# Kernel optimization log

Measured on AMD Instinct MI355X. Metric: run time of the kernel, lower is better.

Reference implementation:

```python
import jax, jax.numpy as jnp
import numpy as np

N_NODES = 40000
N_EDGES = 640000
DIM = 128
N_BASIS = 50
N_FILTERS = 128
CUTOFF = 5.0
LOG2 = float(np.log(2.0))
PI = float(np.pi)


def ssp(t):
    # ShiftedSoftplus: softplus(x) - log(2), numerically stable via logaddexp
    return jnp.logaddexp(t, 0.0) - LOG2


def setup_inputs() -> dict:
    key = jax.random.key(0)
    ks = jax.random.split(key, 16)
    u = lambda k, shape, fan_in: jax.random.uniform(k, shape, jnp.float32, -1.0, 1.0) / np.sqrt(fan_in)
    return {
        "x": jax.random.normal(ks[0], (N_NODES, DIM), jnp.float32),
        "r_ij": jax.random.uniform(ks[1], (N_EDGES,), jnp.float32) * CUTOFF,
        "f_ij": jax.random.normal(ks[2], (N_EDGES, N_BASIS), jnp.float32),
        "ind_i": jax.random.randint(ks[3], (N_EDGES,), 0, N_NODES),
        "ind_j": jax.random.randint(ks[4], (N_EDGES,), 0, N_NODES),
        # parameters
        "W_in2f": u(ks[5], (DIM, N_FILTERS), DIM),            # Linear(dim, n_filters, bias=False)
        "W_f1": u(ks[6], (N_BASIS, N_FILTERS), N_BASIS),       # filter_network Linear 1
        "b_f1": u(ks[7], (N_FILTERS,), N_BASIS),
        "W_f2": u(ks[8], (N_FILTERS, N_FILTERS), N_FILTERS),   # filter_network Linear 2
        "b_f2": u(ks[9], (N_FILTERS,), N_FILTERS),
        "W_out": u(ks[10], (N_FILTERS, DIM), N_FILTERS),       # f2out Linear
        "b_out": u(ks[11], (DIM,), N_FILTERS),
        "W_lin": u(ks[12], (DIM, DIM), DIM),                   # final lin
        "b_lin": u(ks[13], (DIM,), DIM),
    }


def reference(x, r_ij, f_ij, ind_i, ind_j,
              W_in2f, W_f1, b_f1, W_f2, b_f2, W_out, b_out, W_lin, b_lin):
    # filter network: Linear -> ShiftedSoftplus -> Linear, on edges: [E, nf]
    W = ssp(f_ij @ W_f1 + b_f1) @ W_f2 + b_f2
    # cosine cutoff: [E]
    C = 0.5 * (jnp.cos(r_ij * (PI / CUTOFF)) + 1.0) * (r_ij < CUTOFF).astype(r_ij.dtype)
    W = W * C[:, None]
    # node embedding -> filters: [N, nf]
    h = x @ W_in2f
    # gather source nodes, modulate by filters: [E, nf]
    msg = h[ind_j] * W
    # scatter-add pool to destination nodes: [N, nf]
    agg = jax.ops.segment_sum(msg, ind_i, num_segments=x.shape[0])
    # f2out: Linear -> ShiftedSoftplus, then final Linear
    v = ssp(agg @ W_out + b_out)
    return v @ W_lin + b_lin
```

## Files before the change

kernel.cpp:

```cpp
#include <hip/hip_runtime.h>
#include <hip/hip_fp16.h>

#define N_NODES_C 40000
#define N_EDGES_C 640000
#define DIM 128
#define NB 50
#define LDA 132
#define BLK 256
#define TROWS 64
#define LOG2_C 0.6931471805599453f
#define PI_OVER_CUT 0.6283185307179586f
#define NSCAN_BLK 157

typedef __attribute__((ext_vector_type(8))) short s8v;
typedef __attribute__((ext_vector_type(4))) float f4v;

#define MFMA_BF16 __builtin_amdgcn_mfma_f32_16x16x32_bf16

#define SEG_IN2F_H 0
#define SEG_IN2F_L 20480
#define SEG_F1_H   40960
#define SEG_F1_L   51200
#define SEG_F2_H   61440
#define SEG_F2_L   81920
#define SEG_OUT_H  102400
#define SEG_OUT_L  122880
#define SEG_LIN_H  143360
#define SEG_LIN_L  163840
#define WSPLIT_USHORTS 184320

__device__ __forceinline__ unsigned short f2bf(float x) {
    unsigned int u = __float_as_uint(x);
    u += 0x7fffu + ((u >> 16) & 1u);
    return (unsigned short)(u >> 16);
}
__device__ __forceinline__ float bf2f(unsigned short h) {
    return __uint_as_float(((unsigned int)h) << 16);
}
__device__ __forceinline__ float ssp_f(float t) {
    float e = __expf(-fabsf(t));
    return fmaxf(t, 0.0f) + __logf(1.0f + e) - LOG2_C;
}
__device__ __forceinline__ void split8t(const float* av, s8v& Ah, s8v& Al) {
#pragma unroll
    for (int j = 0; j < 8; j += 2) {
        unsigned int u0 = __float_as_uint(av[j]);
        unsigned int u1 = __float_as_uint(av[j + 1]);
        float h0 = __uint_as_float(u0 & 0xffff0000u);
        float h1 = __uint_as_float(u1 & 0xffff0000u);
        unsigned int r0 = __float_as_uint(av[j] - h0);
        unsigned int r1 = __float_as_uint(av[j + 1] - h1);
        ((unsigned int*)&Ah)[j >> 1] = __builtin_amdgcn_perm(u1, u0, 0x07060302);
        ((unsigned int*)&Al)[j >> 1] = __builtin_amdgcn_perm(r1, r0, 0x07060302);
    }
}
__device__ __forceinline__ void mfma4x2(const unsigned short* __restrict__ bh,
                                        const unsigned short* __restrict__ bl,
                                        const s8v& Ah0, const s8v& Al0,
                                        const s8v& Ah1, const s8v& Al1,
                                        f4v acc0[4], f4v acc1[4]) {
    s8v B[4];
#pragma unroll
    for (int t = 0; t < 4; ++t) B[t] = *(const s8v*)(bl + t * 640);
#pragma unroll
    for (int t = 0; t < 4; ++t) {
        acc0[t] = MFMA_BF16(Ah0, B[t], acc0[t], 0, 0, 0);
        acc1[t] = MFMA_BF16(Ah1, B[t], acc1[t], 0, 0, 0);
    }
#pragma unroll
    for (int t = 0; t < 4; ++t) B[t] = *(const s8v*)(bh + t * 640);
#pragma unroll
    for (int t = 0; t < 4; ++t) {
        acc0[t] = MFMA_BF16(Al0, B[t], acc0[t], 0, 0, 0);
        acc0[t] = MFMA_BF16(Ah0, B[t], acc0[t], 0, 0, 0);
        acc1[t] = MFMA_BF16(Al1, B[t], acc1[t], 0, 0, 0);
        acc1[t] = MFMA_BF16(Ah1, B[t], acc1[t], 0, 0, 0);
    }
}

__global__ __launch_bounds__(BLK) void split5_kernel(const float* __restrict__ Wa,
                                                     const float* __restrict__ Wb,
                                                     const float* __restrict__ Wc,
                                                     const float* __restrict__ Wd,
                                                     const float* __restrict__ We,
                                                     unsigned short* __restrict__ Ws) {
    int i = blockIdx.x * BLK + threadIdx.x;
    if (i >= 18 * 4096) return;
    int chunk = i >> 12, r = i & 4095, k = r & 31, col = r >> 5;
    const float* W; int Kr, ck, hb, lb;
    if (chunk < 4)       { W = Wa; Kr = 128; ck = chunk;      hb = SEG_IN2F_H; lb = SEG_IN2F_L; }
    else if (chunk < 6)  { W = Wb; Kr = 50;  ck = chunk - 4;  hb = SEG_F1_H;   lb = SEG_F1_L; }
    else if (chunk < 10) { W = Wc; Kr = 128; ck = chunk - 6;  hb = SEG_F2_H;   lb = SEG_F2_L; }
    else if (chunk < 14) { W = Wd; Kr = 128; ck = chunk - 10; hb = SEG_OUT_H;  lb = SEG_OUT_L; }
    else                 { W = We; Kr = 128; ck = chunk - 14; hb = SEG_LIN_H;  lb = SEG_LIN_L; }
    int krow = ck * 32 + k;
    float v = (krow < Kr) ? W[(size_t)krow * DIM + col] : 0.f;
    unsigned short h16 = f2bf(v);
    int o = ck * 5120 + col * 40 + k;
    Ws[hb + o] = h16;
    Ws[lb + o] = f2bf(v - bf2f(h16));
}

__global__ __launch_bounds__(BLK, 4) void node_in2f_mfma(const float* __restrict__ x,
                                                         const unsigned short* __restrict__ Ws,
                                                         float* __restrict__ h) {
    const int tid = threadIdx.x;
    const int w = tid >> 6, l = tid & 63, lr = l & 15, lk = l >> 4;
    const int rpair = w & 1, colbase = (w >> 1) * 64;
    const int n0 = blockIdx.x * TROWS;
    const int rowA0 = rpair * 32 + lr, rowA1 = rowA0 + 16;
    const float* xr0 = x + (size_t)(n0 + rowA0) * DIM;
    const float* xr1 = x + (size_t)(n0 + rowA1) * DIM;

    f4v acc0[4], acc1[4];
#pragma unroll
    for (int t = 0; t < 4; ++t) {
        acc0[t] = (f4v){0.f, 0.f, 0.f, 0.f};
        acc1[t] = (f4v){0.f, 0.f, 0.f, 0.f};
    }
#pragma unroll
    for (int kc = 0; kc < 4; ++kc) {
        const float* ap0 = xr0 + kc * 32 + lk * 8;
        const float* ap1 = xr1 + kc * 32 + lk * 8;
        float4 a0 = *(const float4*)ap0, a1 = *(const float4*)(ap0 + 4);
        float4 b0 = *(const float4*)ap1, b1 = *(const float4*)(ap1 + 4);
        float av0[8] = {a0.x, a0.y, a0.z, a0.w, a1.x, a1.y, a1.z, a1.w};
        float av1[8] = {b0.x, b0.y, b0.z, b0.w, b1.x, b1.y, b1.z, b1.w};
        s8v Ah0, Al0, Ah1, Al1;
        split8t(av0, Ah0, Al0);
        split8t(av1, Ah1, Al1);
        const int bo = kc * 5120 + (colbase + lr) * 40 + lk * 8;
        mfma4x2(Ws + SEG_IN2F_H + bo, Ws + SEG_IN2F_L + bo, Ah0, Al0, Ah1, Al1, acc0, acc1);
    }
#pragma unroll
    for (int t = 0; t < 4; ++t)
#pragma unroll
        for (int r = 0; r < 4; ++r) {
            int col = colbase + t * 16 + lr;
            h[(size_t)(n0 + rpair * 32 + lk * 4 + r) * DIM + col] = acc0[t][r];
            h[(size_t)(n0 + rpair * 32 + 16 + lk * 4 + r) * DIM + col] = acc1[t][r];
        }
}

__global__ __launch_bounds__(BLK) void hist_kernel(const int* __restrict__ ind_i,
                                                   int* __restrict__ cnt) {
    int e = blockIdx.x * BLK + threadIdx.x;
    if (e < N_EDGES_C) atomicAdd(&cnt[ind_i[e]], 1);
}

__global__ __launch_bounds__(BLK) void scan1_kernel(const int* __restrict__ cnt,
                                                    int* __restrict__ excl,
                                                    int* __restrict__ bsum) {
    __shared__ int s[BLK];
    const int tid = threadIdx.x;
    const int idx = blockIdx.x * BLK + tid;
    int v = (idx < N_NODES_C) ? cnt[idx] : 0;
    s[tid] = v;
    __syncthreads();
    for (int off = 1; off < BLK; off <<= 1) {
        int t = (tid >= off) ? s[tid - off] : 0;
        __syncthreads();
        s[tid] += t;
        __syncthreads();
    }
    if (idx < N_NODES_C) excl[idx] = s[tid] - v;
    if (tid == BLK - 1) bsum[blockIdx.x] = s[tid];
}

__global__ __launch_bounds__(BLK) void scan2_kernel(int* __restrict__ bsum) {
    __shared__ int s[BLK];
    const int tid = threadIdx.x;
    int v = (tid < NSCAN_BLK) ? bsum[tid] : 0;
    s[tid] = v;
    __syncthreads();
    for (int off = 1; off < BLK; off <<= 1) {
        int t = (tid >= off) ? s[tid - off] : 0;
        __syncthreads();
        s[tid] += t;
        __syncthreads();
    }
    if (tid < NSCAN_BLK) bsum[tid] = s[tid] - v;
}

__global__ __launch_bounds__(BLK) void scan3_kernel(int* __restrict__ start,
                                                    int* __restrict__ cursor,
                                                    const int* __restrict__ bsum) {
    const int idx = blockIdx.x * BLK + threadIdx.x;
    if (idx < N_NODES_C) {
        int v = start[idx] + bsum[blockIdx.x];
        start[idx] = v;
        cursor[idx] = v;
    }
}

__global__ __launch_bounds__(BLK) void place_kernel(const int* __restrict__ ind_i,
                                                    int* __restrict__ cursor,
                                                    int* __restrict__ pos) {
    int e = blockIdx.x * BLK + threadIdx.x;
    if (e < N_EDGES_C) {
        int slot = atomicAdd(&cursor[ind_i[e]], 1);
        pos[e] = slot;
    }
}

__global__ __launch_bounds__(BLK, 4) void edge_kernel_mfma(const float* __restrict__ f_ij,
                                                           const float* __restrict__ r_ij,
                                                           const int* __restrict__ ind_j,
                                                           const int* __restrict__ pos,
                                                           const unsigned short* __restrict__ Ws,
                                                           const float* __restrict__ b_f1,
                                                           const float* __restrict__ b_f2,
                                                           const float* __restrict__ h,
                                                           __half* __restrict__ msg) {
    __shared__ __align__(16) char smem[34816];
    unsigned short* t1h = (unsigned short*)smem;
    unsigned short* t1l = t1h + 64 * 136;
    float* tf = (float*)smem;

    const int tid = threadIdx.x;
    const int w = tid >> 6, l = tid & 63, lr = l & 15, lk = l >> 4;
    const int rt = tid >> 4, ct = tid & 15;
    const int rpair = w & 1, colbase = (w >> 1) * 64;
    const int e0 = blockIdx.x * TROWS;
    const int rowA0 = rpair * 32 + lr, rowA1 = rowA0 + 16;

    f4v acc0[4], acc1[4];
#pragma unroll
    for (int t = 0; t < 4; ++t) {
        float bv = b_f1[colbase + t * 16 + lr];
        acc0[t] = (f4v){bv, bv, bv, bv};
        acc1[t] = (f4v){bv, bv, bv, bv};
    }
    const float* fr0 = f_ij + (size_t)(e0 + rowA0) * NB;
    const float* fr1 = f_ij + (size_t)(e0 + rowA1) * NB;
#pragma unroll
    for (int kc = 0; kc < 2; ++kc) {
        int kb = kc * 32 + lk * 8;
        float av0[8], av1[8];
#pragma unroll
        for (int ii = 0; ii < 4; ++ii) {
            int k = kb + ii * 2;
            float2 v0 = (k < NB) ? *(const float2*)(fr0 + k) : make_float2(0.f, 0.f);
            float2 v1 = (k < NB) ? *(const float2*)(fr1 + k) : make_float2(0.f, 0.f);
            av0[ii * 2] = v0.x; av0[ii * 2 + 1] = v0.y;
            av1[ii * 2] = v1.x; av1[ii * 2 + 1] = v1.y;
        }
        s8v Ah0, Al0, Ah1, Al1;
        split8t(av0, Ah0, Al0);
        split8t(av1, Ah1, Al1);
        const int bo = kc * 5120 + (colbase + lr) * 40 + lk * 8;
        mfma4x2(Ws + SEG_F1_H + bo, Ws + SEG_F1_L + bo, Ah0, Al0, Ah1, Al1, acc0, acc1);
    }
#pragma unroll
    for (int t = 0; t < 4; ++t)
#pragma unroll
        for (int r = 0; r < 4; ++r) {
            int col = colbase + t * 16 + lr;
            {
                float v = ssp_f(acc0[t][r]);
                unsigned int u = __float_as_uint(v);
                float hf = __uint_as_float(u & 0xffff0000u);
                int idx = (rpair * 32 + lk * 4 + r) * 136 + col;
                t1h[idx] = (unsigned short)(u >> 16);
                t1l[idx] = (unsigned short)(__float_as_uint(v - hf) >> 16);
            }
            {
                float v = ssp_f(acc1[t][r]);
                unsigned int u = __float_as_uint(v);
                float hf = __uint_as_float(u & 0xffff0000u);
                int idx = (rpair * 32 + 16 + lk * 4 + r) * 136 + col;
                t1h[idx] = (unsigned short)(u >> 16);
                t1l[idx] = (unsigned short)(__float_as_uint(v - hf) >> 16);
            }
        }
    __syncthreads();

#pragma unroll
    for (int t = 0; t < 4; ++t) {
        float bv = b_f2[colbase + t * 16 + lr];
        acc0[t] = (f4v){bv, bv, bv, bv};
        acc1[t] = (f4v){bv, bv, bv, bv};
    }
#pragma unroll
    for (int kc = 0; kc < 4; ++kc) {
        s8v Ah0 = *(const s8v*)&t1h[rowA0 * 136 + kc * 32 + lk * 8];
        s8v Al0 = *(const s8v*)&t1l[rowA0 * 136 + kc * 32 + lk * 8];
        s8v Ah1 = *(const s8v*)&t1h[rowA1 * 136 + kc * 32 + lk * 8];
        s8v Al1 = *(const s8v*)&t1l[rowA1 * 136 + kc * 32 + lk * 8];
        const int bo = kc * 5120 + (colbase + lr) * 40 + lk * 8;
        mfma4x2(Ws + SEG_F2_H + bo, Ws + SEG_F2_L + bo, Ah0, Al0, Ah1, Al1, acc0, acc1);
    }
    __syncthreads();
#pragma unroll
    for (int t = 0; t < 4; ++t)
#pragma unroll
        for (int r = 0; r < 4; ++r) {
            int col = colbase + t * 16 + lr;
            tf[(rpair * 32 + lk * 4 + r) * LDA + col] = acc0[t][r];
            tf[(rpair * 32 + 16 + lk * 4 + r) * LDA + col] = acc1[t][r];
        }
    __syncthreads();

#pragma unroll
    for (int i = 0; i < 4; ++i) {
        int e = e0 + rt * 4 + i;
        float rr = r_ij[e];
        float C = (rr < 5.0f) ? (0.5f * __cosf(rr * PI_OVER_CUT) + 0.5f) : 0.0f;
        int nj = ind_j[e];
        const float* hp = &h[(size_t)nj * DIM + ct * 8];
        float4 h0 = *(const float4*)hp, h1 = *(const float4*)(hp + 4);
        const float* ep = &tf[(rt * 4 + i) * LDA + ct * 8];
        float4 a0 = *(const float4*)ep, a1 = *(const float4*)(ep + 4);
        __half2 o0 = __floats2half2_rn(h0.x * a0.x * C, h0.y * a0.y * C);
        __half2 o1 = __floats2half2_rn(h0.z * a0.z * C, h0.w * a0.w * C);
        __half2 o2 = __floats2half2_rn(h1.x * a1.x * C, h1.y * a1.y * C);
        __half2 o3 = __floats2half2_rn(h1.z * a1.z * C, h1.w * a1.w * C);
        __half* mp = &msg[(size_t)pos[e] * DIM + ct * 8];
        *(uint4*)mp = make_uint4(*(unsigned int*)&o0, *(unsigned int*)&o1,
                                 *(unsigned int*)&o2, *(unsigned int*)&o3);
    }
}

__global__ __launch_bounds__(BLK) void gather_kernel(const __half* __restrict__ msg,
                                                     const int* __restrict__ start,
                                                     const int* __restrict__ cnt,
                                                     float* __restrict__ agg) {
    const int wave = threadIdx.x >> 6;
    const int lane = threadIdx.x & 63;
    const int node = blockIdx.x * 4 + wave;
    if (node >= N_NODES_C) return;
    const int s = start[node];
    const int d = cnt[node];
    const __half* base = msg + (size_t)s * DIM + lane * 2;
    float ax = 0.f, ay = 0.f;
    int k = 0;
    for (; k + 1 < d; k += 2) {
        float2 fa = __half22float2(*(const __half2*)(base + (size_t)k * DIM));
        float2 fb = __half22float2(*(const __half2*)(base + (size_t)(k + 1) * DIM));
        ax += fa.x + fb.x;
        ay += fa.y + fb.y;
    }
    if (k < d) {
        float2 fa = __half22float2(*(const __half2*)(base + (size_t)k * DIM));
        ax += fa.x;
        ay += fa.y;
    }
    *(float2*)&agg[(size_t)node * DIM + lane * 2] = make_float2(ax, ay);
}

__global__ __launch_bounds__(BLK, 4) void node_out_mfma(const float* __restrict__ agg,
                                                        const unsigned short* __restrict__ Ws,
                                                        const float* __restrict__ b_out,
                                                        const float* __restrict__ b_lin,
                                                        float* __restrict__ out) {
    __shared__ __align__(16) char smem[34816];
    unsigned short* t1h = (unsigned short*)smem;
    unsigned short* t1l = t1h + 64 * 136;

    const int tid = threadIdx.x;
    const int w = tid >> 6, l = tid & 63, lr = l & 15, lk = l >> 4;
    const int rpair = w & 1, colbase = (w >> 1) * 64;
    const int n0 = blockIdx.x * TROWS;
    const int rowA0 = rpair * 32 + lr, rowA1 = rowA0 + 16;
    const float* ar0 = agg + (size_t)(n0 + rowA0) * DIM;
    const float* ar1 = agg + (size_t)(n0 + rowA1) * DIM;

    f4v acc0[4], acc1[4];
#pragma unroll
    for (int t = 0; t < 4; ++t) {
        float bv = b_out[colbase + t * 16 + lr];
        acc0[t] = (f4v){bv, bv, bv, bv};
        acc1[t] = (f4v){bv, bv, bv, bv};
    }
#pragma unroll
    for (int kc = 0; kc < 4; ++kc) {
        const float* ap0 = ar0 + kc * 32 + lk * 8;
        const float* ap1 = ar1 + kc * 32 + lk * 8;
        float4 a0 = *(const float4*)ap0, a1 = *(const float4*)(ap0 + 4);
        float4 b0 = *(const float4*)ap1, b1 = *(const float4*)(ap1 + 4);
        float av0[8] = {a0.x, a0.y, a0.z, a0.w, a1.x, a1.y, a1.z, a1.w};
        float av1[8] = {b0.x, b0.y, b0.z, b0.w, b1.x, b1.y, b1.z, b1.w};
        s8v Ah0, Al0, Ah1, Al1;
        split8t(av0, Ah0, Al0);
        split8t(av1, Ah1, Al1);
        const int bo = kc * 5120 + (colbase + lr) * 40 + lk * 8;
        mfma4x2(Ws + SEG_OUT_H + bo, Ws + SEG_OUT_L + bo, Ah0, Al0, Ah1, Al1, acc0, acc1);
    }
#pragma unroll
    for (int t = 0; t < 4; ++t)
#pragma unroll
        for (int r = 0; r < 4; ++r) {
            int col = colbase + t * 16 + lr;
            {
                float v = ssp_f(acc0[t][r]);
                unsigned int u = __float_as_uint(v);
                float hf = __uint_as_float(u & 0xffff0000u);
                int idx = (rpair * 32 + lk * 4 + r) * 136 + col;
                t1h[idx] = (unsigned short)(u >> 16);
                t1l[idx] = (unsigned short)(__float_as_uint(v - hf) >> 16);
            }
            {
                float v = ssp_f(acc1[t][r]);
                unsigned int u = __float_as_uint(v);
                float hf = __uint_as_float(u & 0xffff0000u);
                int idx = (rpair * 32 + 16 + lk * 4 + r) * 136 + col;
                t1h[idx] = (unsigned short)(u >> 16);
                t1l[idx] = (unsigned short)(__float_as_uint(v - hf) >> 16);
            }
        }
    __syncthreads();

#pragma unroll
    for (int t = 0; t < 4; ++t) {
        float bv = b_lin[colbase + t * 16 + lr];
        acc0[t] = (f4v){bv, bv, bv, bv};
        acc1[t] = (f4v){bv, bv, bv, bv};
    }
#pragma unroll
    for (int kc = 0; kc < 4; ++kc) {
        s8v Ah0 = *(const s8v*)&t1h[rowA0 * 136 + kc * 32 + lk * 8];
        s8v Al0 = *(const s8v*)&t1l[rowA0 * 136 + kc * 32 + lk * 8];
        s8v Ah1 = *(const s8v*)&t1h[rowA1 * 136 + kc * 32 + lk * 8];
        s8v Al1 = *(const s8v*)&t1l[rowA1 * 136 + kc * 32 + lk * 8];
        const int bo = kc * 5120 + (colbase + lr) * 40 + lk * 8;
        mfma4x2(Ws + SEG_LIN_H + bo, Ws + SEG_LIN_L + bo, Ah0, Al0, Ah1, Al1, acc0, acc1);
    }
#pragma unroll
    for (int t = 0; t < 4; ++t)
#pragma unroll
        for (int r = 0; r < 4; ++r) {
            int col = colbase + t * 16 + lr;
            out[(size_t)(n0 + rpair * 32 + lk * 4 + r) * DIM + col] = acc0[t][r];
            out[(size_t)(n0 + rpair * 32 + 16 + lk * 4 + r) * DIM + col] = acc1[t][r];
        }
}

__device__ __forceinline__ void stage_chunk(const float* __restrict__ B, int k0, int rows,
                                            float* __restrict__ Bc, int tid) {
    const int n4 = rows * (DIM / 4);
    const float4* Bg = (const float4*)B + (size_t)k0 * (DIM / 4);
    float4* Bc4 = (float4*)Bc;
    for (int i = tid; i < n4; i += BLK) Bc4[i] = Bg[i];
}

__device__ __forceinline__ void init_acc_bias(float acc[4][8], const float* __restrict__ b, int ct) {
    float4 bb0 = *(const float4*)&b[ct * 8];
    float4 bb1 = *(const float4*)&b[ct * 8 + 4];
#pragma unroll
    for (int i = 0; i < 4; ++i) {
        acc[i][0] = bb0.x; acc[i][1] = bb0.y; acc[i][2] = bb0.z; acc[i][3] = bb0.w;
        acc[i][4] = bb1.x; acc[i][5] = bb1.y; acc[i][6] = bb1.z; acc[i][7] = bb1.w;
    }
}

template <int KPAD>
__device__ __forceinline__ void gemm_tile(const float* __restrict__ A_lds, int lda,
                                          const float* __restrict__ Bglob,
                                          float* __restrict__ Bc,
                                          float acc[4][8], int rt, int ct, int tid) {
    for (int k0 = 0; k0 < KPAD; k0 += 32) {
        __syncthreads();
        stage_chunk(Bglob, k0, 32, Bc, tid);
        __syncthreads();
#pragma unroll 2
        for (int k4 = 0; k4 < 8; ++k4) {
            float4 av[4];
#pragma unroll
            for (int i = 0; i < 4; ++i)
                av[i] = *(const float4*)&A_lds[(rt * 4 + i) * lda + k0 + k4 * 4];
#pragma unroll
            for (int kk = 0; kk < 4; ++kk) {
                const float* bp = &Bc[(k4 * 4 + kk) * DIM + ct * 8];
                float4 b0 = *(const float4*)bp;
                float4 b1 = *(const float4*)(bp + 4);
#pragma unroll
                for (int i = 0; i < 4; ++i) {
                    float a = ((const float*)&av[i])[kk];
                    acc[i][0] = fmaf(a, b0.x, acc[i][0]);
                    acc[i][1] = fmaf(a, b0.y, acc[i][1]);
                    acc[i][2] = fmaf(a, b0.z, acc[i][2]);
                    acc[i][3] = fmaf(a, b0.w, acc[i][3]);
                    acc[i][4] = fmaf(a, b1.x, acc[i][4]);
                    acc[i][5] = fmaf(a, b1.y, acc[i][5]);
                    acc[i][6] = fmaf(a, b1.z, acc[i][6]);
                    acc[i][7] = fmaf(a, b1.w, acc[i][7]);
                }
            }
        }
    }
}

template <int NK2>
__device__ __forceinline__ void gemm1_direct(const float* const (&frow)[4], int k2base,
                                             const float* __restrict__ Bc,
                                             float acc[4][8], int ct) {
#pragma unroll 4
    for (int k2 = 0; k2 < NK2; ++k2) {
        float2 a2[4];
#pragma unroll
        for (int i = 0; i < 4; ++i)
            a2[i] = *(const float2*)(frow[i] + (k2base + k2) * 2);
#pragma unroll
        for (int kk = 0; kk < 2; ++kk) {
            const float* bp = &Bc[(k2 * 2 + kk) * DIM + ct * 8];
            float4 b0 = *(const float4*)bp;
            float4 b1 = *(const float4*)(bp + 4);
#pragma unroll
            for (int i = 0; i < 4; ++i) {
                float a = kk ? a2[i].y : a2[i].x;
                acc[i][0] = fmaf(a, b0.x, acc[i][0]);
                acc[i][1] = fmaf(a, b0.y, acc[i][1]);
                acc[i][2] = fmaf(a, b0.z, acc[i][2]);
                acc[i][3] = fmaf(a, b0.w, acc[i][3]);
                acc[i][4] = fmaf(a, b1.x, acc[i][4]);
                acc[i][5] = fmaf(a, b1.y, acc[i][5]);
                acc[i][6] = fmaf(a, b1.z, acc[i][6]);
                acc[i][7] = fmaf(a, b1.w, acc[i][7]);
            }
        }
    }
}

__global__ __launch_bounds__(BLK) void node_in2f_fb(const float* __restrict__ x,
                                                    const float* __restrict__ W,
                                                    float* __restrict__ h) {
    __shared__ float At[TROWS * LDA];
    __shared__ float Bc[32 * DIM];
    const int tid = threadIdx.x;
    const int rt = tid >> 4, ct = tid & 15;
    const int n0 = blockIdx.x * TROWS;
    for (int i = tid; i < TROWS * (DIM / 4); i += BLK) {
        int row = i >> 5, c4 = i & 31;
        *(float4*)&At[row * LDA + c4 * 4] = *(const float4*)&x[(size_t)(n0 + row) * DIM + c4 * 4];
    }
    float acc[4][8];
#pragma unroll
    for (int i = 0; i < 4; ++i)
#pragma unroll
        for (int j = 0; j < 8; ++j) acc[i][j] = 0.f;
    gemm_tile<DIM>(At, LDA, W, Bc, acc, rt, ct, tid);
#pragma unroll
    for (int i = 0; i < 4; ++i) {
        float* hp = &h[(size_t)(n0 + rt * 4 + i) * DIM + ct * 8];
        *(float4*)hp = make_float4(acc[i][0], acc[i][1], acc[i][2], acc[i][3]);
        *(float4*)(hp + 4) = make_float4(acc[i][4], acc[i][5], acc[i][6], acc[i][7]);
    }
}

__global__ __launch_bounds__(BLK) void node_out_fb(const float* __restrict__ agg,
                                                   const float* __restrict__ W_out,
                                                   const float* __restrict__ b_out,
                                                   const float* __restrict__ W_lin,
                                                   const float* __restrict__ b_lin,
                                                   float* __restrict__ out) {
    __shared__ float At[TROWS * LDA];
    __shared__ float Bc[32 * DIM];
    const int tid = threadIdx.x;
    const int rt = tid >> 4, ct = tid & 15;
    const int n0 = blockIdx.x * TROWS;
    for (int i = tid; i < TROWS * (DIM / 4); i += BLK) {
        int row = i >> 5, c4 = i & 31;
        *(float4*)&At[row * LDA + c4 * 4] = *(const float4*)&agg[(size_t)(n0 + row) * DIM + c4 * 4];
    }
    float acc[4][8];
    init_acc_bias(acc, b_out, ct);
    gemm_tile<DIM>(At, LDA, W_out, Bc, acc, rt, ct, tid);
    __syncthreads();
#pragma unroll
    for (int i = 0; i < 4; ++i) {
        float* tp = &At[(rt * 4 + i) * LDA + ct * 8];
        *(float4*)tp = make_float4(ssp_f(acc[i][0]), ssp_f(acc[i][1]),
                                   ssp_f(acc[i][2]), ssp_f(acc[i][3]));
        *(float4*)(tp + 4) = make_float4(ssp_f(acc[i][4]), ssp_f(acc[i][5]),
                                         ssp_f(acc[i][6]), ssp_f(acc[i][7]));
    }
    init_acc_bias(acc, b_lin, ct);
    gemm_tile<DIM>(At, LDA, W_lin, Bc, acc, rt, ct, tid);
#pragma unroll
    for (int i = 0; i < 4; ++i) {
        float* op = &out[(size_t)(n0 + rt * 4 + i) * DIM + ct * 8];
        *(float4*)op = make_float4(acc[i][0], acc[i][1], acc[i][2], acc[i][3]);
        *(float4*)(op + 4) = make_float4(acc[i][4], acc[i][5], acc[i][6], acc[i][7]);
    }
}

__global__ __launch_bounds__(BLK) void edge_kernel_atomic(const float* __restrict__ f_ij,
                                                          const float* __restrict__ r_ij,
                                                          const int* __restrict__ ind_i,
                                                          const int* __restrict__ ind_j,
                                                          const float* __restrict__ W_f1,
                                                          const float* __restrict__ b_f1,
                                                          const float* __restrict__ W_f2,
                                                          const float* __restrict__ b_f2,
                                                          const float* __restrict__ h,
                                                          float* __restrict__ agg) {
    __shared__ float t1[TROWS * LDA];
    __shared__ float Bc[32 * DIM];
    const int tid = threadIdx.x;
    const int rt = tid >> 4, ct = tid & 15;
    const int e0 = blockIdx.x * TROWS;
    const float* frow[4];
#pragma unroll
    for (int i = 0; i < 4; ++i) frow[i] = f_ij + (size_t)(e0 + rt * 4 + i) * NB;
    float acc[4][8];
    init_acc_bias(acc, b_f1, ct);
    stage_chunk(W_f1, 0, 32, Bc, tid);
    __syncthreads();
    gemm1_direct<16>(frow, 0, Bc, acc, ct);
    __syncthreads();
    stage_chunk(W_f1, 32, 18, Bc, tid);
    __syncthreads();
    gemm1_direct<9>(frow, 16, Bc, acc, ct);
#pragma unroll
    for (int i = 0; i < 4; ++i) {
        float* tp = &t1[(rt * 4 + i) * LDA + ct * 8];
        *(float4*)tp = make_float4(ssp_f(acc[i][0]), ssp_f(acc[i][1]),
                                   ssp_f(acc[i][2]), ssp_f(acc[i][3]));
        *(float4*)(tp + 4) = make_float4(ssp_f(acc[i][4]), ssp_f(acc[i][5]),
                                         ssp_f(acc[i][6]), ssp_f(acc[i][7]));
    }
    init_acc_bias(acc, b_f2, ct);
    gemm_tile<DIM>(t1, LDA, W_f2, Bc, acc, rt, ct, tid);
#pragma unroll
    for (int i = 0; i < 4; ++i) {
        int e = e0 + rt * 4 + i;
        float r = r_ij[e];
        float C = (r < 5.0f) ? 0.5f * (cosf(r * PI_OVER_CUT) + 1.0f) : 0.0f;
        int nj = ind_j[e];
        int ni = ind_i[e];
        const float* hp = &h[(size_t)nj * DIM + ct * 8];
        float4 h0 = *(const float4*)hp;
        float4 h1 = *(const float4*)(hp + 4);
        float* ap = &agg[(size_t)ni * DIM + ct * 8];
        atomicAdd(ap + 0, h0.x * acc[i][0] * C);
        atomicAdd(ap + 1, h0.y * acc[i][1] * C);
        atomicAdd(ap + 2, h0.z * acc[i][2] * C);
        atomicAdd(ap + 3, h0.w * acc[i][3] * C);
        atomicAdd(ap + 4, h1.x * acc[i][4] * C);
        atomicAdd(ap + 5, h1.y * acc[i][5] * C);
        atomicAdd(ap + 6, h1.z * acc[i][6] * C);
        atomicAdd(ap + 7, h1.w * acc[i][7] * C);
    }
}

extern "C" void kernel_launch(void* const* d_in, const int* in_sizes, int n_in,
                              void* d_out, int out_size, void* d_ws, size_t ws_size,
                              hipStream_t stream) {
    const float* x      = (const float*)d_in[0];
    const float* r_ij   = (const float*)d_in[1];
    const float* f_ij   = (const float*)d_in[2];
    const int*   ind_i  = (const int*)d_in[3];
    const int*   ind_j  = (const int*)d_in[4];
    const float* W_in2f = (const float*)d_in[5];
    const float* W_f1   = (const float*)d_in[6];
    const float* b_f1   = (const float*)d_in[7];
    const float* W_f2   = (const float*)d_in[8];
    const float* b_f2   = (const float*)d_in[9];
    const float* W_out  = (const float*)d_in[10];
    const float* b_out  = (const float*)d_in[11];
    const float* W_lin  = (const float*)d_in[12];
    const float* b_lin  = (const float*)d_in[13];
    float* out = (float*)d_out;

    char* ws = (char*)d_ws;
    size_t off = 0;
    auto alloc = [&](size_t bytes) {
        char* p = ws + off;
        off = (off + bytes + 511) & ~(size_t)511;
        return p;
    };
    unsigned short* Wsplit = (unsigned short*)alloc(WSPLIT_USHORTS * sizeof(unsigned short));
    float*  h      = (float*)alloc((size_t)N_NODES_C * DIM * sizeof(float));
    float*  agg    = (float*)alloc((size_t)N_NODES_C * DIM * sizeof(float));
    __half* msg    = (__half*)alloc((size_t)N_EDGES_C * DIM * sizeof(__half));
    int*    pos    = (int*)alloc((size_t)N_EDGES_C * sizeof(int));
    int*    cnt    = (int*)alloc((size_t)N_NODES_C * sizeof(int));
    int*    startA = (int*)alloc((size_t)N_NODES_C * sizeof(int));
    int*    cursor = (int*)alloc((size_t)N_NODES_C * sizeof(int));
    int*    bsum   = (int*)alloc((size_t)NSCAN_BLK * sizeof(int));
    const bool have_ws = (off <= ws_size);

    if (have_ws) {
        split5_kernel<<<(18 * 4096 + BLK - 1) / BLK, BLK, 0, stream>>>(
            W_in2f, W_f1, W_f2, W_out, W_lin, Wsplit);

        node_in2f_mfma<<<N_NODES_C / TROWS, BLK, 0, stream>>>(x, Wsplit, h);

        hipMemsetAsync(cnt, 0, (size_t)N_NODES_C * sizeof(int), stream);
        hist_kernel<<<(N_EDGES_C + BLK - 1) / BLK, BLK, 0, stream>>>(ind_i, cnt);
        scan1_kernel<<<NSCAN_BLK, BLK, 0, stream>>>(cnt, startA, bsum);
        scan2_kernel<<<1, BLK, 0, stream>>>(bsum);
        scan3_kernel<<<NSCAN_BLK, BLK, 0, stream>>>(startA, cursor, bsum);
        place_kernel<<<(N_EDGES_C + BLK - 1) / BLK, BLK, 0, stream>>>(ind_i, cursor, pos);

        edge_kernel_mfma<<<N_EDGES_C / TROWS, BLK, 0, stream>>>(
            f_ij, r_ij, ind_j, pos, Wsplit, b_f1, b_f2, h, msg);
        gather_kernel<<<(N_NODES_C + 3) / 4, BLK, 0, stream>>>(msg, startA, cnt, agg);

        node_out_mfma<<<N_NODES_C / TROWS, BLK, 0, stream>>>(agg, Wsplit, b_out, b_lin, out);
    } else {
        float* h2   = (float*)d_ws;
        float* agg2 = h2 + (size_t)N_NODES_C * DIM;
        node_in2f_fb<<<N_NODES_C / TROWS, BLK, 0, stream>>>(x, W_in2f, h2);
        hipMemsetAsync(agg2, 0, (size_t)N_NODES_C * DIM * sizeof(float), stream);
        edge_kernel_atomic<<<N_EDGES_C / TROWS, BLK, 0, stream>>>(
            f_ij, r_ij, ind_i, ind_j, W_f1, b_f1, W_f2, b_f2, h2, agg2);
        node_out_fb<<<N_NODES_C / TROWS, BLK, 0, stream>>>(agg2, W_out, b_out, W_lin, b_lin, out);
    }
}
```

Before: 308.4 us.

## Fuse gather into node output kernel and software-pipeline B loads in edge GEMMs

Removes the separate gather kernel and the fp32 agg buffer. The node output kernel now sums each node's fp16 messages directly into LDS as split bf16 tiles and then runs both GEMMs on them. The edge kernel double-buffers the weight fragment loads across k-chunks and issues the r_ij, ind_j, pos and h gathers earlier so they overlap with the MFMA work. The cost is higher register pressure and a gather loop inside a GEMM kernel, where 16 threads serialize each node's message sum and degree imbalance can stall the block.

Result: faster. 298.4 us (-3.2%).

```diff
diff --git a/kernel.cpp b/kernel.cpp
--- a/kernel.cpp
+++ b/kernel.cpp
@@ -54,28 +54,101 @@
         ((unsigned int*)&Al)[j >> 1] = __builtin_amdgcn_perm(r1, r0, 0x07060302);
     }
 }
+__device__ __forceinline__ void f2x4_to_split(const float2 v[4], s8v& Ah, s8v& Al) {
+    float av[8] = {v[0].x, v[0].y, v[1].x, v[1].y, v[2].x, v[2].y, v[3].x, v[3].y};
+    split8t(av, Ah, Al);
+}
+__device__ __forceinline__ void loadB4(const unsigned short* __restrict__ p, s8v B[4]) {
+#pragma unroll
+    for (int t = 0; t < 4; ++t) B[t] = *(const s8v*)(p + t * 640);
+}
+__device__ __forceinline__ void mfma8_half(const s8v B[4], const s8v& A0, const s8v& A1,
+                                           f4v acc0[4], f4v acc1[4]) {
+#pragma unroll
+    for (int t = 0; t < 4; ++t) {
+        acc0[t] = MFMA_BF16(A0, B[t], acc0[t], 0, 0, 0);
+        acc1[t] = MFMA_BF16(A1, B[t], acc1[t], 0, 0, 0);
+    }
+}
+__device__ __forceinline__ void mfma16_half(const s8v B[4], const s8v& Ah0, const s8v& Al0,
+                                            const s8v& Ah1, const s8v& Al1,
+                                            f4v acc0[4], f4v acc1[4]) {
+#pragma unroll
+    for (int t = 0; t < 4; ++t) {
+        acc0[t] = MFMA_BF16(Al0, B[t], acc0[t], 0, 0, 0);
+        acc0[t] = MFMA_BF16(Ah0, B[t], acc0[t], 0, 0, 0);
+        acc1[t] = MFMA_BF16(Al1, B[t], acc1[t], 0, 0, 0);
+        acc1[t] = MFMA_BF16(Ah1, B[t], acc1[t], 0, 0, 0);
+    }
+}
 __device__ __forceinline__ void mfma4x2(const unsigned short* __restrict__ bh,
                                         const unsigned short* __restrict__ bl,
                                         const s8v& Ah0, const s8v& Al0,
                                         const s8v& Ah1, const s8v& Al1,
                                         f4v acc0[4], f4v acc1[4]) {
     s8v B[4];
-#pragma unroll
-    for (int t = 0; t < 4; ++t) B[t] = *(const s8v*)(bl + t * 640);
+    loadB4(bl, B);
+    mfma8_half(B, Ah0, Ah1, acc0, acc1);
+    loadB4(bh, B);
+    mfma16_half(B, Ah0, Al0, Ah1, Al1, acc0, acc1);
+}
+__device__ __forceinline__ void init_acc_cols(f4v acc0[4], f4v acc1[4],
+                                              const float* __restrict__ b, int colbase, int lr) {
 #pragma unroll
     for (int t = 0; t < 4; ++t) {
-        acc0[t] = MFMA_BF16(Ah0, B[t], acc0[t], 0, 0, 0);
-        acc1[t] = MFMA_BF16(Ah1, B[t], acc1[t], 0, 0, 0);
-    }
-#pragma unroll
-    for (int t = 0; t < 4; ++t) B[t] = *(const s8v*)(bh + t * 640);
-#pragma unroll
-    for (int t = 0; t < 4; ++t) {
-        acc0[t] = MFMA_BF16(Al0, B[t], acc0[t], 0, 0, 0);
-        acc0[t] = MFMA_BF16(Ah0, B[t], acc0[t], 0, 0, 0);
-        acc1[t] = MFMA_BF16(Al1, B[t], acc1[t], 0, 0, 0);
-        acc1[t] = MFMA_BF16(Ah1, B[t], acc1[t], 0, 0, 0);
-    }
+        float bv = b[colbase + t * 16 + lr];
+        acc0[t] = (f4v){bv, bv, bv, bv};
+        acc1[t] = (f4v){bv, bv, bv, bv};
+    }
+}
+__device__ __forceinline__ void gemm_lds_ws(const unsigned short* __restrict__ t1h,
+                                            const unsigned short* __restrict__ t1l,
+                                            int rowA0, int rowA1, int lk,
+                                            const unsigned short* __restrict__ bh,
+                                            const unsigned short* __restrict__ bl,
+                                            f4v acc0[4], f4v acc1[4]) {
+    s8v BlA[4], BhA[4], BlB[4], BhB[4];
+    loadB4(bl, BlA);
+    loadB4(bh, BhA);
+#define KC_STEP(K, BL, BH, BLN, BHN, LOADNEXT)                                 \
+    {                                                                          \
+        s8v Ah0 = *(const s8v*)&t1h[rowA0 * 136 + (K) * 32 + lk * 8];          \
+        s8v Al0 = *(const s8v*)&t1l[rowA0 * 136 + (K) * 32 + lk * 8];          \
+        s8v Ah1 = *(const s8v*)&t1h[rowA1 * 136 + (K) * 32 + lk * 8];          \
+        s8v Al1 = *(const s8v*)&t1l[rowA1 * 136 + (K) * 32 + lk * 8];          \
+        mfma8_half(BL, Ah0, Ah1, acc0, acc1);                                  \
+        if (LOADNEXT) loadB4(bl + ((K) + 1) * 5120, BLN);                      \
+        mfma16_half(BH, Ah0, Al0, Ah1, Al1, acc0, acc1);                       \
+        if (LOADNEXT) loadB4(bh + ((K) + 1) * 5120, BHN);                      \
+    }
+    KC_STEP(0, BlA, BhA, BlB, BhB, true)
+    KC_STEP(1, BlB, BhB, BlA, BhA, true)
+    KC_STEP(2, BlA, BhA, BlB, BhB, true)
+    KC_STEP(3, BlB, BhB, BlA, BhA, false)
+#undef KC_STEP
+}
+__device__ __forceinline__ void store_t1_ssp(const f4v acc0[4], const f4v acc1[4],
+                                             unsigned short* __restrict__ t1h,
+                                             unsigned short* __restrict__ t1l,
+                                             int rpair, int colbase, int lk, int lr) {
+#pragma unroll
+    for (int t = 0; t < 4; ++t)
+#pragma unroll
+        for (int r = 0; r < 4; ++r) {
+            int col = colbase + t * 16 + lr;
+            float v = ssp_f(acc0[t][r]);
+            unsigned int u = __float_as_uint(v);
+            float hf = __uint_as_float(u & 0xffff0000u);
+            int idx = (rpair * 32 + lk * 4 + r) * 136 + col;
+            t1h[idx] = (unsigned short)(u >> 16);
+            t1l[idx] = (unsigned short)(__float_as_uint(v - hf) >> 16);
+            v = ssp_f(acc1[t][r]);
+            u = __float_as_uint(v);
+            hf = __uint_as_float(u & 0xffff0000u);
+            idx = (rpair * 32 + 16 + lk * 4 + r) * 136 + col;
+            t1h[idx] = (unsigned short)(u >> 16);
+            t1l[idx] = (unsigned short)(__float_as_uint(v - hf) >> 16);
+        }
 }
 
 __global__ __launch_bounds__(BLK) void split5_kernel(const float* __restrict__ Wa,
@@ -223,72 +296,66 @@
     const int rpair = w & 1, colbase = (w >> 1) * 64;
     const int e0 = blockIdx.x * TROWS;
     const int rowA0 = rpair * 32 + lr, rowA1 = rowA0 + 16;
-
-    f4v acc0[4], acc1[4];
-#pragma unroll
-    for (int t = 0; t < 4; ++t) {
-        float bv = b_f1[colbase + t * 16 + lr];
-        acc0[t] = (f4v){bv, bv, bv, bv};
-        acc1[t] = (f4v){bv, bv, bv, bv};
-    }
+    const int boff = (colbase + lr) * 40 + lk * 8;
+
     const float* fr0 = f_ij + (size_t)(e0 + rowA0) * NB;
     const float* fr1 = f_ij + (size_t)(e0 + rowA1) * NB;
-#pragma unroll
-    for (int kc = 0; kc < 2; ++kc) {
-        int kb = kc * 32 + lk * 8;
-        float av0[8], av1[8];
+    float2 fv[2][2][4];
+#pragma unroll
+    for (int kc = 0; kc < 2; ++kc)
 #pragma unroll
         for (int ii = 0; ii < 4; ++ii) {
-            int k = kb + ii * 2;
-            float2 v0 = (k < NB) ? *(const float2*)(fr0 + k) : make_float2(0.f, 0.f);
-            float2 v1 = (k < NB) ? *(const float2*)(fr1 + k) : make_float2(0.f, 0.f);
-            av0[ii * 2] = v0.x; av0[ii * 2 + 1] = v0.y;
-            av1[ii * 2] = v1.x; av1[ii * 2 + 1] = v1.y;
-        }
-        s8v Ah0, Al0, Ah1, Al1;
-        split8t(av0, Ah0, Al0);
-        split8t(av1, Ah1, Al1);
-        const int bo = kc * 5120 + (colbase + lr) * 40 + lk * 8;
-        mfma4x2(Ws + SEG_F1_H + bo, Ws + SEG_F1_L + bo, Ah0, Al0, Ah1, Al1, acc0, acc1);
-    }
-#pragma unroll
-    for (int t = 0; t < 4; ++t)
-#pragma unroll
-        for (int r = 0; r < 4; ++r) {
-            int col = colbase + t * 16 + lr;
-            {
-                float v = ssp_f(acc0[t][r]);
-                unsigned int u = __float_as_uint(v);
-                float hf = __uint_as_float(u & 0xffff0000u);
-                int idx = (rpair * 32 + lk * 4 + r) * 136 + col;
-                t1h[idx] = (unsigned short)(u >> 16);
-                t1l[idx] = (unsigned short)(__float_as_uint(v - hf) >> 16);
-            }
-            {
-                float v = ssp_f(acc1[t][r]);
-                unsigned int u = __float_as_uint(v);
-                float hf = __uint_as_float(u & 0xffff0000u);
-                int idx = (rpair * 32 + 16 + lk * 4 + r) * 136 + col;
-                t1h[idx] = (unsigned short)(u >> 16);
-                t1l[idx] = (unsigned short)(__float_as_uint(v - hf) >> 16);
-            }
-        }
-    __syncthreads();
-
-#pragma unroll
-    for (int t = 0; t < 4; ++t) {
-        float bv = b_f2[colbase + t * 16 + lr];
-        acc0[t] = (f4v){bv, bv, bv, bv};
-        acc1[t] = (f4v){bv, bv, bv, bv};
-    }
-#pragma unroll
-    for (int kc = 0; kc < 4; ++kc) {
-        s8v Ah0 = *(const s8v*)&t1h[rowA0 * 136 + kc * 32 + lk * 8];
-        s8v Al0 = *(const s8v*)&t1l[rowA0 * 136 + kc * 32 + lk * 8];
-        s8v Ah1 = *(const s8v*)&t1h[rowA1 * 136 + kc * 32 + lk * 8];
-        s8v Al1 = *(const s8v*)&t1l[rowA1 * 136 + kc * 32 + lk * 8];
-        const int bo = kc * 5120 + (colbase + lr) * 40 + lk * 8;
-        mfma4x2(Ws + SEG_F2_H + bo, Ws + SEG_F2_L + bo, Ah0, Al0, Ah1, Al1, acc0, acc1);
+            int k = kc * 32 + lk * 8 + ii * 2;
+            fv[kc][0][ii] = (k < NB) ? *(const float2*)(fr0 + k) : make_float2(0.f, 0.f);
+            fv[kc][1][ii] = (k < NB) ? *(const float2*)(fr1 + k) : make_float2(0.f, 0.f);
+        }
+
+    f4v acc0[4], acc1[4];
+    init_acc_cols(acc0, acc1, b_f1, colbase, lr);
+    const unsigned short* f1h = Ws + SEG_F1_H + boff;
+    const unsigned short* f1l = Ws + SEG_F1_L + boff;
+    {
+        s8v BlA[4], BhA[4], BlB[4], BhB[4];
+        loadB4(f1l, BlA);
+        loadB4(f1h, BhA);
+        {
+            s8v Ah0, Al0, Ah1, Al1;
+            f2x4_to_split(fv[0][0], Ah0, Al0);
+            f2x4_to_split(fv[0][1], Ah1, Al1);
+            mfma8_half(BlA, Ah0, Ah1, acc0, acc1);
+            loadB4(f1l + 5120, BlB);
+            mfma16_half(BhA, Ah0, Al0, Ah1, Al1, acc0, acc1);
+            loadB4(f1h + 5120, BhB);
+        }
+        {
+            s8v Ah0, Al0, Ah1, Al1;
+            f2x4_to_split(fv[1][0], Ah0, Al0);
+            f2x4_to_split(fv[1][1], Ah1, Al1);
+            mfma8_half(BlB, Ah0, Ah1, acc0, acc1);
+            mfma16_half(BhB, Ah0, Al0, Ah1, Al1, acc0, acc1);
+        }
+    }
+    store_t1_ssp(acc0, acc1, t1h, t1l, rpair, colbase, lk, lr);
+    float rr4[4]; int nj4[4], ps4[4];
+#pragma unroll
+    for (int i = 0; i < 4; ++i) {
+        int e = e0 + rt * 4 + i;
+        rr4[i] = r_ij[e];
+        nj4[i] = ind_j[e];
+        ps4[i] = pos[e];
+    }
+    __syncthreads();
+
+    init_acc_cols(acc0, acc1, b_f2, colbase, lr);
+    gemm_lds_ws(t1h, t1l, rowA0, rowA1, lk,
+                Ws + SEG_F2_H + boff, Ws + SEG_F2_L + boff, acc0, acc1);
+
+    float4 hv[4][2];
+#pragma unroll
+    for (int i = 0; i < 4; ++i) {
+        const float* hp = &h[(size_t)nj4[i] * DIM + ct * 8];
+        hv[i][0] = *(const float4*)hp;
+        hv[i][1] = *(const float4*)(hp + 4);
     }
     __syncthreads();
 #pragma unroll
@@ -303,56 +370,27 @@
 
 #pragma unroll
     for (int i = 0; i < 4; ++i) {
-        int e = e0 + rt * 4 + i;
-        float rr = r_ij[e];
-        float C = (rr < 5.0f) ? (0.5f * __cosf(rr * PI_OVER_CUT) + 0.5f) : 0.0f;
-        int nj = ind_j[e];
-        const float* hp = &h[(size_t)nj * DIM + ct * 8];
-        float4 h0 = *(const float4*)hp, h1 = *(const float4*)(hp + 4);
+        float C = (rr4[i] < 5.0f) ? (0.5f * __cosf(rr4[i] * PI_OVER_CUT) + 0.5f) : 0.0f;
         const float* ep = &tf[(rt * 4 + i) * LDA + ct * 8];
         float4 a0 = *(const float4*)ep, a1 = *(const float4*)(ep + 4);
+        float4 h0 = hv[i][0], h1 = hv[i][1];
         __half2 o0 = __floats2half2_rn(h0.x * a0.x * C, h0.y * a0.y * C);
         __half2 o1 = __floats2half2_rn(h0.z * a0.z * C, h0.w * a0.w * C);
         __half2 o2 = __floats2half2_rn(h1.x * a1.x * C, h1.y * a1.y * C);
         __half2 o3 = __floats2half2_rn(h1.z * a1.z * C, h1.w * a1.w * C);
-        __half* mp = &msg[(size_t)pos[e] * DIM + ct * 8];
+        __half* mp = &msg[(size_t)ps4[i] * DIM + ct * 8];
         *(uint4*)mp = make_uint4(*(unsigned int*)&o0, *(unsigned int*)&o1,
                                  *(unsigned int*)&o2, *(unsigned int*)&o3);
     }
 }
 
-__global__ __launch_bounds__(BLK) void gather_kernel(const __half* __restrict__ msg,
-                                                     const int* __restrict__ start,
-                                                     const int* __restrict__ cnt,
-                                                     float* __restrict__ agg) {
-    const int wave = threadIdx.x >> 6;
-    const int lane = threadIdx.x & 63;
-    const int node = blockIdx.x * 4 + wave;
-    if (node >= N_NODES_C) return;
-    const int s = start[node];
-    const int d = cnt[node];
-    const __half* base = msg + (size_t)s * DIM + lane * 2;
-    float ax = 0.f, ay = 0.f;
-    int k = 0;
-    for (; k + 1 < d; k += 2) {
-        float2 fa = __half22float2(*(const __half2*)(base + (size_t)k * DIM));
-        float2 fb = __half22float2(*(const __half2*)(base + (size_t)(k + 1) * DIM));
-        ax += fa.x + fb.x;
-        ay += fa.y + fb.y;
-    }
-    if (k < d) {
-        float2 fa = __half22float2(*(const __half2*)(base + (size_t)k * DIM));
-        ax += fa.x;
-        ay += fa.y;
-    }
-    *(float2*)&agg[(size_t)node * DIM + lane * 2] = make_float2(ax, ay);
-}
-
-__global__ __launch_bounds__(BLK, 4) void node_out_mfma(const float* __restrict__ agg,
-                                                        const unsigned short* __restrict__ Ws,
-                                                        const float* __restrict__ b_out,
-                                                        const float* __restrict__ b_lin,
-                                                        float* __restrict__ out) {
+__global__ __launch_bounds__(BLK, 4) void node_out_fused(const __half* __restrict__ msg,
+                                                         const int* __restrict__ start,
+                                                         const int* __restrict__ cnt,
+                                                         const unsigned short* __restrict__ Ws,
+                                                         const float* __restrict__ b_out,
+                                                         const float* __restrict__ b_lin,
+                                                         float* __restrict__ out) {
     __shared__ __align__(16) char smem[34816];
     unsigned short* t1h = (unsigned short*)smem;
     unsigned short* t1l = t1h + 64 * 136;
@@ -362,69 +400,45 @@
     const int rpair = w & 1, colbase = (w >> 1) * 64;
     const int n0 = blockIdx.x * TROWS;
     const int rowA0 = rpair * 32 + lr, rowA1 = rowA0 + 16;
-    const float* ar0 = agg + (size_t)(n0 + rowA0) * DIM;
-    const float* ar1 = agg + (size_t)(n0 + rowA1) * DIM;
+    const int boff = (colbase + lr) * 40 + lk * 8;
+
+    const int q = tid >> 4, l16 = tid & 15;
+#pragma unroll
+    for (int i = 0; i < 4; ++i) {
+        int nrow = q * 4 + i;
+        int node = n0 + nrow;
+        int s = start[node];
+        int d = cnt[node];
+        float a[8] = {0.f, 0.f, 0.f, 0.f, 0.f, 0.f, 0.f, 0.f};
+        const __half* bp = msg + (size_t)s * DIM + l16 * 8;
+        for (int k = 0; k < d; ++k) {
+            uint4 v = *(const uint4*)(bp + (size_t)k * DIM);
+            const __half2* hp2 = (const __half2*)&v;
+#pragma unroll
+            for (int j = 0; j < 4; ++j) {
+                float2 f = __half22float2(hp2[j]);
+                a[j * 2] += f.x;
+                a[j * 2 + 1] += f.y;
+            }
+        }
+        s8v Ah, Al;
+        split8t(a, Ah, Al);
+        *(s8v*)&t1h[nrow * 136 + l16 * 8] = Ah;
+        *(s8v*)&t1l[nrow * 136 + l16 * 8] = Al;
+    }
+    __syncthreads();
 
     f4v acc0[4], acc1[4];
-#pragma unroll
-    for (int t = 0; t < 4; ++t) {
-        float bv = b_out[colbase + t * 16 + lr];
-        acc0[t] = (f4v){bv, bv, bv, bv};
-        acc1[t] = (f4v){bv, bv, bv, bv};
-    }
-#pragma unroll
-    for (int kc = 0; kc < 4; ++kc) {
-        const float* ap0 = ar0 + kc * 32 + lk * 8;
-        const float* ap1 = ar1 + kc * 32 + lk * 8;
-        float4 a0 = *(const float4*)ap0, a1 = *(const float4*)(ap0 + 4);
-        float4 b0 = *(const float4*)ap1, b1 = *(const float4*)(ap1 + 4);
-        float av0[8] = {a0.x, a0.y, a0.z, a0.w, a1.x, a1.y, a1.z, a1.w};
-        float av1[8] = {b0.x, b0.y, b0.z, b0.w, b1.x, b1.y, b1.z, b1.w};
-        s8v Ah0, Al0, Ah1, Al1;
-        split8t(av0, Ah0, Al0);
-        split8t(av1, Ah1, Al1);
-        const int bo = kc * 5120 + (colbase + lr) * 40 + lk * 8;
-        mfma4x2(Ws + SEG_OUT_H + bo, Ws + SEG_OUT_L + bo, Ah0, Al0, Ah1, Al1, acc0, acc1);
-    }
-#pragma unroll
-    for (int t = 0; t < 4; ++t)
-#pragma unroll
-        for (int r = 0; r < 4; ++r) {
-            int col = colbase + t * 16 + lr;
-            {
-                float v = ssp_f(acc0[t][r]);
-                unsigned int u = __float_as_uint(v);
-                float hf = __uint_as_float(u & 0xffff0000u);
-                int idx = (rpair * 32 + lk * 4 + r) * 136 + col;
-                t1h[idx] = (unsigned short)(u >> 16);
-                t1l[idx] = (unsigned short)(__float_as_uint(v - hf) >> 16);
-            }
-            {
-                float v = ssp_f(acc1[t][r]);
-                unsigned int u = __float_as_uint(v);
-                float hf = __uint_as_float(u & 0xffff0000u);
-                int idx = (rpair * 32 + 16 + lk * 4 + r) * 136 + col;
-                t1h[idx] = (unsigned short)(u >> 16);
-                t1l[idx] = (unsigned short)(__float_as_uint(v - hf) >> 16);
-            }
-        }
-    __syncthreads();
-
-#pragma unroll
-    for (int t = 0; t < 4; ++t) {
-        float bv = b_lin[colbase + t * 16 + lr];
-        acc0[t] = (f4v){bv, bv, bv, bv};
-        acc1[t] = (f4v){bv, bv, bv, bv};
-    }
-#pragma unroll
-    for (int kc = 0; kc < 4; ++kc) {
-        s8v Ah0 = *(const s8v*)&t1h[rowA0 * 136 + kc * 32 + lk * 8];
-        s8v Al0 = *(const s8v*)&t1l[rowA0 * 136 + kc * 32 + lk * 8];
-        s8v Ah1 = *(const s8v*)&t1h[rowA1 * 136 + kc * 32 + lk * 8];
-        s8v Al1 = *(const s8v*)&t1l[rowA1 * 136 + kc * 32 + lk * 8];
-        const int bo = kc * 5120 + (colbase + lr) * 40 + lk * 8;
-        mfma4x2(Ws + SEG_LIN_H + bo, Ws + SEG_LIN_L + bo, Ah0, Al0, Ah1, Al1, acc0, acc1);
-    }
+    init_acc_cols(acc0, acc1, b_out, colbase, lr);
+    gemm_lds_ws(t1h, t1l, rowA0, rowA1, lk,
+                Ws + SEG_OUT_H + boff, Ws + SEG_OUT_L + boff, acc0, acc1);
+    __syncthreads();
+    store_t1_ssp(acc0, acc1, t1h, t1l, rpair, colbase, lk, lr);
+    __syncthreads();
+
+    init_acc_cols(acc0, acc1, b_lin, colbase, lr);
+    gemm_lds_ws(t1h, t1l, rowA0, rowA1, lk,
+                Ws + SEG_LIN_H + boff, Ws + SEG_LIN_L + boff, acc0, acc1);
 #pragma unroll
     for (int t = 0; t < 4; ++t)
 #pragma unroll
@@ -671,7 +685,6 @@
     };
     unsigned short* Wsplit = (unsigned short*)alloc(WSPLIT_USHORTS * sizeof(unsigned short));
     float*  h      = (float*)alloc((size_t)N_NODES_C * DIM * sizeof(float));
-    float*  agg    = (float*)alloc((size_t)N_NODES_C * DIM * sizeof(float));
     __half* msg    = (__half*)alloc((size_t)N_EDGES_C * DIM * sizeof(__half));
     int*    pos    = (int*)alloc((size_t)N_EDGES_C * sizeof(int));
     int*    cnt    = (int*)alloc((size_t)N_NODES_C * sizeof(int));
@@ -695,9 +708,9 @@
 
         edge_kernel_mfma<<<N_EDGES_C / TROWS, BLK, 0, stream>>>(
             f_ij, r_ij, ind_j, pos, Wsplit, b_f1, b_f2, h, msg);
-        gather_kernel<<<(N_NODES_C + 3) / 4, BLK, 0, stream>>>(msg, startA, cnt, agg);
-
-        node_out_mfma<<<N_NODES_C / TROWS, BLK, 0, stream>>>(agg, Wsplit, b_out, b_lin, out);
+
+        node_out_fused<<<N_NODES_C / TROWS, BLK, 0, stream>>>(
+            msg, startA, cnt, Wsplit, b_out, b_lin, out);
     } else {
         float* h2   = (float*)d_ws;
         float* agg2 = h2 + (size_t)N_NODES_C * DIM;
```
